# Performance work log

Hardware: AMD Instinct MI355X
Metric: run time of the kernel (lower is better)

Reference implementation:

```python
import jax, jax.numpy as jnp
import numpy as np

N_NODES = 100000
N_EDGES = 1600000
T = 24
F_IN = 16
H = 128
OUT = 64


def setup_inputs() -> dict:
    key = jax.random.key(0)
    ks = jax.random.split(key, 12)
    s = 0.05
    return {
        "x_time_series": jax.random.normal(ks[0], (N_NODES, T, F_IN), jnp.float32),
        "edge_index": jax.random.randint(ks[1], (2, N_EDGES), 0, N_NODES, jnp.int64),
        "gru_W_ih": jax.random.normal(ks[2], (3 * H, F_IN), jnp.float32) * s,
        "gru_W_hh": jax.random.normal(ks[3], (3 * H, H), jnp.float32) * s,
        "gru_b_ih": jax.random.normal(ks[4], (3 * H,), jnp.float32) * s,
        "gru_b_hh": jax.random.normal(ks[5], (3 * H,), jnp.float32) * s,
        "lin1_l_W": jax.random.normal(ks[6], (H, H), jnp.float32) * s,
        "lin1_l_b": jax.random.normal(ks[7], (H,), jnp.float32) * s,
        "lin1_r_W": jax.random.normal(ks[8], (H, H), jnp.float32) * s,
        "lin2_l_W": jax.random.normal(ks[9], (OUT, H), jnp.float32) * s,
        "lin2_l_b": jax.random.normal(ks[10], (OUT,), jnp.float32) * s,
        "lin2_r_W": jax.random.normal(ks[11], (OUT, H), jnp.float32) * s,
    }


def gru_last(x, W_ih, W_hh, b_ih, b_hh):
    # x: [N, T, F]; single-layer batch_first GRU, return last hidden state [N, H]
    Hd = W_hh.shape[1]
    # precompute input projections for all steps: [T, N, 3H]
    gi_all = jnp.einsum('ntf,gf->tng', x, W_ih) + b_ih

    def step(h, gi):
        gh = h @ W_hh.T + b_hh
        r = jax.nn.sigmoid(gi[:, :Hd] + gh[:, :Hd])
        z = jax.nn.sigmoid(gi[:, Hd:2 * Hd] + gh[:, Hd:2 * Hd])
        n = jnp.tanh(gi[:, 2 * Hd:] + r * gh[:, 2 * Hd:])
        h_new = (1.0 - z) * n + z * h
        return h_new, None

    h0 = jnp.zeros((x.shape[0], Hd), x.dtype)
    h_last, _ = jax.lax.scan(step, h0, gi_all)
    return h_last


def sage_conv(x, edge_index, W_l, b_l, W_r):
    # PyG SAGEConv with mean aggregation:
    #   out_i = W_l @ mean_{j->i} x_j + b_l + W_r @ x_i
    src, dst = edge_index[0], edge_index[1]
    n = x.shape[0]
    msg = x[src]                                   # [E, F] irregular gather
    agg = jax.ops.segment_sum(msg, dst, num_segments=n)
    cnt = jax.ops.segment_sum(jnp.ones((msg.shape[0],), x.dtype), dst, num_segments=n)
    mean = agg / jnp.maximum(cnt, 1.0)[:, None]
    return mean @ W_l.T + b_l + x @ W_r.T


def reference(x_time_series, edge_index, gru_W_ih, gru_W_hh, gru_b_ih, gru_b_hh,
              lin1_l_W, lin1_l_b, lin1_r_W, lin2_l_W, lin2_l_b, lin2_r_W):
    x = x_time_series.reshape(-1, T, F_IN)
    h = gru_last(x, gru_W_ih, gru_W_hh, gru_b_ih, gru_b_hh)   # [N, H]
    g = sage_conv(h, edge_index, lin1_l_W, lin1_l_b, lin1_r_W) + h
    g = jax.nn.relu(g)
    # dropout in eval mode -> identity
    out = sage_conv(g, edge_index, lin2_l_W, lin2_l_b, lin2_r_W)
    return out
```

## Files before the change

kernel.cpp:

```cpp
#include <hip/hip_runtime.h>
#include <math.h>

#define NND 100000
#define TT 24
#define FI 16
#define HD 128
#define GD 384
#define OD 64
#define NE 1600000

typedef __bf16 bf16x8 __attribute__((ext_vector_type(8)));
typedef float f32x4 __attribute__((ext_vector_type(4)));
typedef unsigned short u16;
typedef unsigned int u32;

#define S_RZ (-1.44269504f)
#define S_N  (-2.88539008f)

__device__ __forceinline__ u16 f2b(float f) {
    u32 u = __float_as_uint(f);
    u32 r = (u + 0x7FFFu + ((u >> 16) & 1u)) >> 16;
    return (u16)r;
}
__device__ __forceinline__ u32 cvtpk(float lo, float hi) {
    u32 r;
    asm("v_cvt_pk_bf16_f32 %0, %1, %2" : "=v"(r) : "v"(lo), "v"(hi));
    return r;
}
__device__ __forceinline__ float b2f(u16 v) {
    return __uint_as_float((u32)v << 16);
}

__global__ void cvt_x_kernel(const float* __restrict__ x, u16* __restrict__ xb) {
    size_t base = ((size_t)blockIdx.x * 256 + threadIdx.x) * 8;
    float4 a = *(const float4*)(x + base);
    float4 b = *(const float4*)(x + base + 4);
    u32 o0 = cvtpk(a.x, a.y), o1 = cvtpk(a.z, a.w);
    u32 o2 = cvtpk(b.x, b.y), o3 = cvtpk(b.z, b.w);
    *(uint4*)(xb + base) = make_uint4(o0, o1, o2, o3);
}

__global__ void pack_w_kernel(const float* __restrict__ Whh, const float* __restrict__ Wih,
                              const float* __restrict__ bih, const float* __restrict__ bhh,
                              u16* __restrict__ Ap, u16* __restrict__ Aip) {
    int id = blockIdx.x * 256 + threadIdx.x;
    if (id < 6144) {
        int lane = id & 63, fs = id >> 6;
        int s = fs & 3, gt = fs >> 2;
        int row = gt * 16 + (lane & 15);
        float sc = (row < 2 * HD) ? S_RZ : S_N;
        int k0 = s * 32 + (lane >> 4) * 8;
        const float* src = Whh + (size_t)row * HD + k0;
        u16 o[8];
#pragma unroll
        for (int e = 0; e < 8; ++e) o[e] = f2b(src[e] * sc);
        u32* dst = (u32*)(Ap + (size_t)id * 8);
#pragma unroll
        for (int e = 0; e < 4; ++e) dst[e] = (u32)o[2 * e] | ((u32)o[2 * e + 1] << 16);
    } else if (id < 7680) {
        int id2 = id - 6144;
        int lane = id2 & 63, gt = id2 >> 6;
        int row = gt * 16 + (lane & 15);
        float sc = (row < 2 * HD) ? S_RZ : S_N;
        int g = lane >> 4;
        u16 o[8] = {0, 0, 0, 0, 0, 0, 0, 0};
        if (g < 2) {
            const float* src = Wih + (size_t)row * FI + g * 8;
#pragma unroll
            for (int e = 0; e < 8; ++e) o[e] = f2b(src[e] * sc);
        } else if (g == 2) {
            float bias = (row < 2 * HD) ? (bih[row] + bhh[row]) : bih[row];
            o[0] = f2b(bias * sc);
        }
        u32* dst = (u32*)(Aip + (size_t)id2 * 8);
#pragma unroll
        for (int e = 0; e < 4; ++e) dst[e] = (u32)o[2 * e] | ((u32)o[2 * e + 1] << 16);
    }
}

__global__ void pack_gemm_kernel(const float* __restrict__ W, u16* __restrict__ F, int rows) {
    int id = blockIdx.x * 256 + threadIdx.x;
    if (id >= rows * 16) return;
    int lane = id & 63, fs = id >> 6;
    int s = fs & 3, tile = fs >> 2;
    int row = tile * 16 + (lane & 15);
    int k0 = s * 32 + (lane >> 4) * 8;
    const float* src = W + (size_t)row * HD + k0;
    u16 o[8];
#pragma unroll
    for (int e = 0; e < 8; ++e) o[e] = f2b(src[e]);
    u32* dst = (u32*)(F + (size_t)id * 8);
#pragma unroll
    for (int e = 0; e < 4; ++e) dst[e] = (u32)o[2 * e] | ((u32)o[2 * e + 1] << 16);
}

__device__ __forceinline__ int hidx(int row, int col) {
    return row * 128 + (col ^ ((row & 7) << 3));
}

__global__ __launch_bounds__(512) void gru_mfma_kernel(
    const u16* __restrict__ xb,
    const u16* __restrict__ Ap,
    const u16* __restrict__ Aip,
    const float* __restrict__ bhh,
    const u16* __restrict__ Wl,
    const u16* __restrict__ Wr,
    const float* __restrict__ b1,
    u16* __restrict__ P16,
    float* __restrict__ q)
{
    __shared__ u16 hb0[64 * 128];
    __shared__ u16 hb1[64 * 128];

    const int tid = threadIdx.x;
    const int w = tid >> 6, lane = tid & 63;
    const int l15 = lane & 15, g = lane >> 4;
    const int gbase = blockIdx.x * 64;
    const int j0 = w * 16 + g * 4;

    for (int i = tid; i < 64 * 128 / 2; i += 512) ((u32*)hb0)[i] = 0u;

    bf16x8 Ah[3][4], Ai[3];
#pragma unroll
    for (int a = 0; a < 3; ++a) {
        int gt = w + a * 8;
#pragma unroll
        for (int s = 0; s < 4; ++s)
            Ah[a][s] = *(const bf16x8*)(Ap + ((size_t)(gt * 4 + s) * 64 + lane) * 8);
        Ai[a] = *(const bf16x8*)(Aip + ((size_t)gt * 64 + lane) * 8);
    }

    f32x4 bnh4 = *(const f32x4*)(bhh + 256 + j0);
#pragma unroll
    for (int r = 0; r < 4; ++r) bnh4[r] *= S_N;

    const f32x4 fz = {0.f, 0.f, 0.f, 0.f};
    bf16x8 xdef;
    {
        uint4 u = make_uint4(0u, 0u, 0u, 0u);
        if (g == 2) u.x = 0x3F80u;
        *(uint4*)&xdef = u;
    }

    f32x4 hreg[4];
#pragma unroll
    for (int m = 0; m < 4; ++m) hreg[m] = fz;

    int xoff[4];
#pragma unroll
    for (int m = 0; m < 4; ++m) {
        int nd = gbase + m * 16 + l15;
        nd = nd < NND ? nd : NND - 1;
        xoff[m] = nd * (TT * FI) + g * 8;
    }

    __syncthreads();

    auto dostep = [&](int t, const u16* __restrict__ rb, u16* __restrict__ wb) {
#pragma unroll
        for (int mh = 0; mh < 2; ++mh) {
            const int ma = mh * 2, mb = mh * 2 + 1;
            bf16x8 xf0 = xdef, xf1 = xdef;
            if (g < 2) {
                xf0 = *(const bf16x8*)(xb + (size_t)(xoff[ma] + t * FI));
                xf1 = *(const bf16x8*)(xb + (size_t)(xoff[mb] + t * FI));
            }

            const int ra = ma * 16 + l15, rbr = mb * 16 + l15;
            bf16x8 b0[4], b1f[4];
#pragma unroll
            for (int s = 0; s < 4; ++s) {
                b0[s]  = *(const bf16x8*)&rb[hidx(ra, s * 32 + g * 8)];
                b1f[s] = *(const bf16x8*)&rb[hidx(rbr, s * 32 + g * 8)];
            }

            f32x4 acc[3][2], acci[2];
#pragma unroll
            for (int a = 0; a < 3; ++a) {
                acc[a][0] = __builtin_amdgcn_mfma_f32_16x16x32_bf16(Ah[a][0], b0[0], fz, 0, 0, 0);
                acc[a][1] = __builtin_amdgcn_mfma_f32_16x16x32_bf16(Ah[a][0], b1f[0], fz, 0, 0, 0);
            }
#pragma unroll
            for (int s = 1; s < 4; ++s) {
#pragma unroll
                for (int a = 0; a < 3; ++a) {
                    acc[a][0] = __builtin_amdgcn_mfma_f32_16x16x32_bf16(Ah[a][s], b0[s], acc[a][0], 0, 0, 0);
                    acc[a][1] = __builtin_amdgcn_mfma_f32_16x16x32_bf16(Ah[a][s], b1f[s], acc[a][1], 0, 0, 0);
                }
            }
            acc[0][0] = __builtin_amdgcn_mfma_f32_16x16x32_bf16(Ai[0], xf0, acc[0][0], 0, 0, 0);
            acc[1][0] = __builtin_amdgcn_mfma_f32_16x16x32_bf16(Ai[1], xf0, acc[1][0], 0, 0, 0);
            acci[0]   = __builtin_amdgcn_mfma_f32_16x16x32_bf16(Ai[2], xf0, fz, 0, 0, 0);
            acc[0][1] = __builtin_amdgcn_mfma_f32_16x16x32_bf16(Ai[0], xf1, acc[0][1], 0, 0, 0);
            acc[1][1] = __builtin_amdgcn_mfma_f32_16x16x32_bf16(Ai[1], xf1, acc[1][1], 0, 0, 0);
            acci[1]   = __builtin_amdgcn_mfma_f32_16x16x32_bf16(Ai[2], xf1, fz, 0, 0, 0);

#pragma unroll
            for (int mi = 0; mi < 2; ++mi) {
                int m = mh * 2 + mi;
#pragma unroll
                for (int r = 0; r < 4; ++r) {
                    float rr = __builtin_amdgcn_rcpf(1.0f + __builtin_amdgcn_exp2f(acc[0][mi][r]));
                    float zz = __builtin_amdgcn_rcpf(1.0f + __builtin_amdgcn_exp2f(acc[1][mi][r]));
                    float na = acci[mi][r] + rr * (acc[2][mi][r] + bnh4[r]);
                    float nn = 2.0f * __builtin_amdgcn_rcpf(1.0f + __builtin_amdgcn_exp2f(na)) - 1.0f;
                    float h = nn + zz * (hreg[m][r] - nn);
                    hreg[m][r] = h;
                }
                u32 p0 = cvtpk(hreg[m][0], hreg[m][1]);
                u32 p1 = cvtpk(hreg[m][2], hreg[m][3]);
                *(uint2*)&wb[hidx(m * 16 + l15, j0)] = make_uint2(p0, p1);
            }
        }
        __syncthreads();
    };

#pragma unroll 1
    for (int tt = 0; tt < TT; tt += 2) {
        dostep(tt, hb0, hb1);
        dostep(tt + 1, hb1, hb0);
    }

    bf16x8 Al[4], Ar[4];
#pragma unroll
    for (int s = 0; s < 4; ++s) {
        Al[s] = *(const bf16x8*)(Wl + ((size_t)(w * 4 + s) * 64 + lane) * 8);
        Ar[s] = *(const bf16x8*)(Wr + ((size_t)(w * 4 + s) * 64 + lane) * 8);
    }
    f32x4 bq = *(const f32x4*)(b1 + j0);

#pragma unroll
    for (int m = 0; m < 4; ++m) {
        bf16x8 b[4];
#pragma unroll
        for (int s = 0; s < 4; ++s)
            b[s] = *(const bf16x8*)&hb0[hidx(m * 16 + l15, s * 32 + g * 8)];
        f32x4 ap = fz, aq = fz;
#pragma unroll
        for (int s = 0; s < 4; ++s) {
            ap = __builtin_amdgcn_mfma_f32_16x16x32_bf16(Al[s], b[s], ap, 0, 0, 0);
            aq = __builtin_amdgcn_mfma_f32_16x16x32_bf16(Ar[s], b[s], aq, 0, 0, 0);
        }
        int nd = gbase + m * 16 + l15;
        if (nd < NND) {
            u32 c0 = cvtpk(ap[0], ap[1]), c1 = cvtpk(ap[2], ap[3]);
            *(uint2*)(P16 + (size_t)nd * HD + j0) = make_uint2(c0, c1);
            f32x4 v = aq + bq + hreg[m];
            *(f32x4*)(q + (size_t)nd * HD + j0) = v;
        }
    }
}

__global__ void count_kernel(const int* __restrict__ dst, int* __restrict__ cnt) {
    int e = blockIdx.x * 256 + threadIdx.x;
    if (e < NE) atomicAdd(&cnt[dst[e]], 1);
}

__global__ void blocksum_kernel(const int* __restrict__ cnt, int* __restrict__ bsum) {
    __shared__ int sh[256];
    int b = blockIdx.x, t = threadIdx.x;
    int base = b * 1024;
    int s = 0;
    for (int i = t; i < 1024; i += 256) {
        int idx = base + i;
        s += (idx < NND) ? cnt[idx] : 0;
    }
    sh[t] = s; __syncthreads();
    for (int o = 128; o > 0; o >>= 1) { if (t < o) sh[t] += sh[t + o]; __syncthreads(); }
    if (t == 0) bsum[b] = sh[0];
}

__global__ void scanbsum_kernel(int* __restrict__ bsum, int nb, int* __restrict__ rowptr) {
    if (threadIdx.x == 0 && blockIdx.x == 0) {
        int acc = 0;
        for (int i = 0; i < nb; ++i) { int v = bsum[i]; bsum[i] = acc; acc += v; }
        rowptr[NND] = NE;
    }
}

__global__ void scan_kernel(const int* __restrict__ cnt, const int* __restrict__ bsum,
                            int* __restrict__ rowptr) {
    __shared__ int sh[256];
    int b = blockIdx.x, t = threadIdx.x;
    int base = b * 1024;
    int v[4], loc = 0;
#pragma unroll
    for (int j = 0; j < 4; ++j) {
        int idx = base + t * 4 + j;
        v[j] = (idx < NND) ? cnt[idx] : 0;
        loc += v[j];
    }
    sh[t] = loc; __syncthreads();
    for (int o = 1; o < 256; o <<= 1) {
        int x = (t >= o) ? sh[t - o] : 0;
        __syncthreads();
        sh[t] += x;
        __syncthreads();
    }
    int acc = bsum[b] + sh[t] - loc;
#pragma unroll
    for (int j = 0; j < 4; ++j) {
        int idx = base + t * 4 + j;
        if (idx < NND) rowptr[idx] = acc;
        acc += v[j];
    }
}

__global__ void fill_kernel(const int* __restrict__ src, const int* __restrict__ dst,
                            const int* __restrict__ rowptr, int* __restrict__ fill,
                            int* __restrict__ csr) {
    int e = blockIdx.x * 256 + threadIdx.x;
    if (e >= NE) return;
    int d = dst[e];
    int pos = rowptr[d] + atomicAdd(&fill[d], 1);
    csr[pos] = src[e];
}

__global__ __launch_bounds__(512) void gather_proj_kernel(
    const u16* __restrict__ P16,
    const int* __restrict__ rowptr, const int* __restrict__ csr,
    const float* __restrict__ q,
    const u16* __restrict__ W2l, const u16* __restrict__ W2r,
    const float* __restrict__ b2,
    u16* __restrict__ P2,
    float* __restrict__ q2)
{
    __shared__ u16 xs[64 * 128];

    const int tid = threadIdx.x;
    const int w = tid >> 6, lane = tid & 63;
    const int l15 = lane & 15, g = lane >> 4;
    const int gbase = blockIdx.x * 64;
    const f32x4 fz = {0.f, 0.f, 0.f, 0.f};

#pragma unroll 1
    for (int i = 0; i < 8; ++i) {
        int nloc = w * 8 + i;
        int n = gbase + nloc;
        u32 gv = 0u;
        if (n < NND) {
            int beg = rowptr[n], end = rowptr[n + 1];
            float ax = 0.f, ay = 0.f;
            for (int cb = beg; cb < end; cb += 64) {
                int myi = (cb + lane < end) ? csr[cb + lane] : 0;
                int nn = min(end - cb, 64);
                for (int ii = 0; ii < nn; ++ii) {
                    int s = __shfl(myi, ii);
                    u32 pv = *(const u32*)(P16 + (size_t)s * HD + lane * 2);
                    ax += b2f((u16)pv); ay += b2f((u16)(pv >> 16));
                }
            }
            int deg = end - beg;
            float inv = 1.0f / (float)(deg > 0 ? deg : 1);
            float2 qv = *(const float2*)(q + (size_t)n * HD + lane * 2);
            gv = cvtpk(fmaxf(ax * inv + qv.x, 0.f), fmaxf(ay * inv + qv.y, 0.f));
        }
        *(u32*)&xs[hidx(nloc, lane * 2)] = gv;
    }
    __syncthreads();

    const int tile = w & 3;
    const bool isQ = (w >= 4);
    const u16* Wsel = isQ ? W2r : W2l;
    bf16x8 A[4];
#pragma unroll
    for (int s = 0; s < 4; ++s)
        A[s] = *(const bf16x8*)(Wsel + ((size_t)(tile * 4 + s) * 64 + lane) * 8);
    const int f0 = tile * 16 + g * 4;
    f32x4 bq = *(const f32x4*)(b2 + f0);

#pragma unroll
    for (int m = 0; m < 4; ++m) {
        bf16x8 b[4];
#pragma unroll
        for (int s = 0; s < 4; ++s)
            b[s] = *(const bf16x8*)&xs[hidx(m * 16 + l15, s * 32 + g * 8)];
        f32x4 a = fz;
#pragma unroll
        for (int s = 0; s < 4; ++s)
            a = __builtin_amdgcn_mfma_f32_16x16x32_bf16(A[s], b[s], a, 0, 0, 0);
        int nd = gbase + m * 16 + l15;
        if (nd < NND) {
            if (isQ) {
                f32x4 v = a + bq;
                *(f32x4*)(q2 + (size_t)nd * OD + f0) = v;
            } else {
                u32 c0 = cvtpk(a[0], a[1]), c1 = cvtpk(a[2], a[3]);
                *(uint2*)(P2 + (size_t)nd * OD + f0) = make_uint2(c0, c1);
            }
        }
    }
}

__global__ __launch_bounds__(256) void gather2_kernel(
    const u16* __restrict__ P2,
    const int* __restrict__ rowptr, const int* __restrict__ csr,
    const float* __restrict__ q2,
    float* __restrict__ outp)
{
    int n = ((blockIdx.x * 256 + threadIdx.x) >> 6);
    if (n >= NND) return;
    int lane = threadIdx.x & 63;
    int beg = rowptr[n], end = rowptr[n + 1];

    float a = 0.f;
    for (int cb = beg; cb < end; cb += 64) {
        int myi = (cb + lane < end) ? csr[cb + lane] : 0;
        int nn = min(end - cb, 64);
        for (int i = 0; i < nn; ++i) {
            int s = __shfl(myi, i);
            a += b2f(P2[(size_t)s * OD + lane]);
        }
    }
    int deg = end - beg;
    float inv = 1.0f / (float)(deg > 0 ? deg : 1);
    outp[(size_t)n * OD + lane] = a * inv + q2[(size_t)n * OD + lane];
}

extern "C" void kernel_launch(void* const* d_in, const int* in_sizes, int n_in,
                              void* d_out, int out_size, void* d_ws, size_t ws_size,
                              hipStream_t stream) {
    const float* x   = (const float*)d_in[0];
    const int*   edg = (const int*)d_in[1];
    const int*   src = edg;
    const int*   dst = edg + NE;
    const float* Wih = (const float*)d_in[2];
    const float* Whh = (const float*)d_in[3];
    const float* bih = (const float*)d_in[4];
    const float* bhh = (const float*)d_in[5];
    const float* W1l = (const float*)d_in[6];
    const float* b1  = (const float*)d_in[7];
    const float* W1r = (const float*)d_in[8];
    const float* W2l = (const float*)d_in[9];
    const float* b2  = (const float*)d_in[10];
    const float* W2r = (const float*)d_in[11];
    float* out = (float*)d_out;

    char* wsp = (char*)d_ws;
    auto alloc = [&](size_t nbytes) {
        char* p = wsp; wsp += (nbytes + 255) & ~(size_t)255; return p;
    };
    u16*   Ap    = (u16*)alloc((size_t)6144 * 8 * 2);
    u16*   Aip   = (u16*)alloc((size_t)1536 * 8 * 2);
    u16*   Pw1l  = (u16*)alloc((size_t)2048 * 8 * 2);
    u16*   Pw1r  = (u16*)alloc((size_t)2048 * 8 * 2);
    u16*   Pw2l  = (u16*)alloc((size_t)1024 * 8 * 2);
    u16*   Pw2r  = (u16*)alloc((size_t)1024 * 8 * 2);
    int*   cnt   = (int*)alloc((size_t)NND * 4);
    int*   fill  = (int*)alloc((size_t)NND * 4);
    int*   rowp  = (int*)alloc((size_t)(NND + 1) * 4);
    int*   bsum  = (int*)alloc((size_t)128 * 4);
    int*   csr   = (int*)alloc((size_t)NE * 4);
    u16*   xb    = (u16*)alloc((size_t)NND * TT * FI * 2);
    float* q     = (float*)alloc((size_t)NND * HD * 4);
    u16*   P16   = (u16*)alloc((size_t)NND * HD * 2);
    u16*   P2    = (u16*)alloc((size_t)NND * OD * 2);
    float* q2    = (float*)alloc((size_t)NND * OD * 4);

    const int NB_SCAN = (NND + 1023) / 1024;

    hipMemsetAsync(cnt, 0, (size_t)NND * 4, stream);
    hipMemsetAsync(fill, 0, (size_t)NND * 4, stream);

    cvt_x_kernel<<<(NND * TT * FI) / (256 * 8), 256, 0, stream>>>(x, xb);
    pack_w_kernel<<<30, 256, 0, stream>>>(Whh, Wih, bih, bhh, Ap, Aip);
    pack_gemm_kernel<<<8, 256, 0, stream>>>(W1l, Pw1l, HD);
    pack_gemm_kernel<<<8, 256, 0, stream>>>(W1r, Pw1r, HD);
    pack_gemm_kernel<<<4, 256, 0, stream>>>(W2l, Pw2l, OD);
    pack_gemm_kernel<<<4, 256, 0, stream>>>(W2r, Pw2r, OD);

    count_kernel<<<(NE + 255) / 256, 256, 0, stream>>>(dst, cnt);
    blocksum_kernel<<<NB_SCAN, 256, 0, stream>>>(cnt, bsum);
    scanbsum_kernel<<<1, 64, 0, stream>>>(bsum, NB_SCAN, rowp);
    scan_kernel<<<NB_SCAN, 256, 0, stream>>>(cnt, bsum, rowp);
    fill_kernel<<<(NE + 255) / 256, 256, 0, stream>>>(src, dst, rowp, fill, csr);

    const int nblk = (NND + 63) / 64;
    gru_mfma_kernel<<<nblk, 512, 0, stream>>>(xb, Ap, Aip, bhh, Pw1l, Pw1r, b1, P16, q);

    gather_proj_kernel<<<nblk, 512, 0, stream>>>(P16, rowp, csr, q, Pw2l, Pw2r, b2, P2, q2);

    gather2_kernel<<<(NND * 64 + 255) / 256, 256, 0, stream>>>(P2, rowp, csr, q2, out);
}
```

Measured before the change: 831.9 us.

## Restructure GRU step per row tile, batch gather loads, reuse count array for CSR fill

The GRU step now processes one 16-row tile at a time instead of two paired tiles, and the final projection loads each B fragment inside the MFMA loop. Both changes are meant to lower register pressure, at the cost of less instruction-level parallelism per step. The two neighbour-gather kernels issue eight independent loads before accumulating, to hide memory latency in the irregular gather. The CSR fill now decrements the existing count array with atomicSub instead of using a separate zeroed fill array, which removes one memset and one buffer. The order of neighbours within each row changes as a result, so the bf16 summation order also changes.

```diff
diff --git a/kernel.cpp b/kernel.cpp
--- a/kernel.cpp
+++ b/kernel.cpp
@@ -158,59 +158,42 @@
 
     auto dostep = [&](int t, const u16* __restrict__ rb, u16* __restrict__ wb) {
 #pragma unroll
-        for (int mh = 0; mh < 2; ++mh) {
-            const int ma = mh * 2, mb = mh * 2 + 1;
-            bf16x8 xf0 = xdef, xf1 = xdef;
-            if (g < 2) {
-                xf0 = *(const bf16x8*)(xb + (size_t)(xoff[ma] + t * FI));
-                xf1 = *(const bf16x8*)(xb + (size_t)(xoff[mb] + t * FI));
-            }
-
-            const int ra = ma * 16 + l15, rbr = mb * 16 + l15;
-            bf16x8 b0[4], b1f[4];
-#pragma unroll
-            for (int s = 0; s < 4; ++s) {
-                b0[s]  = *(const bf16x8*)&rb[hidx(ra, s * 32 + g * 8)];
-                b1f[s] = *(const bf16x8*)&rb[hidx(rbr, s * 32 + g * 8)];
-            }
-
-            f32x4 acc[3][2], acci[2];
-#pragma unroll
-            for (int a = 0; a < 3; ++a) {
-                acc[a][0] = __builtin_amdgcn_mfma_f32_16x16x32_bf16(Ah[a][0], b0[0], fz, 0, 0, 0);
-                acc[a][1] = __builtin_amdgcn_mfma_f32_16x16x32_bf16(Ah[a][0], b1f[0], fz, 0, 0, 0);
+        for (int m = 0; m < 4; ++m) {
+            bf16x8 xf = xdef;
+            if (g < 2)
+                xf = *(const bf16x8*)(xb + (size_t)(xoff[m] + t * FI));
+
+            const int row = m * 16 + l15;
+            f32x4 a0, a1, a2, ai;
+            {
+                bf16x8 b = *(const bf16x8*)&rb[hidx(row, g * 8)];
+                a0 = __builtin_amdgcn_mfma_f32_16x16x32_bf16(Ah[0][0], b, fz, 0, 0, 0);
+                a1 = __builtin_amdgcn_mfma_f32_16x16x32_bf16(Ah[1][0], b, fz, 0, 0, 0);
+                a2 = __builtin_amdgcn_mfma_f32_16x16x32_bf16(Ah[2][0], b, fz, 0, 0, 0);
             }
 #pragma unroll
             for (int s = 1; s < 4; ++s) {
-#pragma unroll
-                for (int a = 0; a < 3; ++a) {
-                    acc[a][0] = __builtin_amdgcn_mfma_f32_16x16x32_bf16(Ah[a][s], b0[s], acc[a][0], 0, 0, 0);
-                    acc[a][1] = __builtin_amdgcn_mfma_f32_16x16x32_bf16(Ah[a][s], b1f[s], acc[a][1], 0, 0, 0);
-                }
-            }
-            acc[0][0] = __builtin_amdgcn_mfma_f32_16x16x32_bf16(Ai[0], xf0, acc[0][0], 0, 0, 0);
-            acc[1][0] = __builtin_amdgcn_mfma_f32_16x16x32_bf16(Ai[1], xf0, acc[1][0], 0, 0, 0);
-            acci[0]   = __builtin_amdgcn_mfma_f32_16x16x32_bf16(Ai[2], xf0, fz, 0, 0, 0);
-            acc[0][1] = __builtin_amdgcn_mfma_f32_16x16x32_bf16(Ai[0], xf1, acc[0][1], 0, 0, 0);
-            acc[1][1] = __builtin_amdgcn_mfma_f32_16x16x32_bf16(Ai[1], xf1, acc[1][1], 0, 0, 0);
-            acci[1]   = __builtin_amdgcn_mfma_f32_16x16x32_bf16(Ai[2], xf1, fz, 0, 0, 0);
-
-#pragma unroll
-            for (int mi = 0; mi < 2; ++mi) {
-                int m = mh * 2 + mi;
-#pragma unroll
-                for (int r = 0; r < 4; ++r) {
-                    float rr = __builtin_amdgcn_rcpf(1.0f + __builtin_amdgcn_exp2f(acc[0][mi][r]));
-                    float zz = __builtin_amdgcn_rcpf(1.0f + __builtin_amdgcn_exp2f(acc[1][mi][r]));
-                    float na = acci[mi][r] + rr * (acc[2][mi][r] + bnh4[r]);
-                    float nn = 2.0f * __builtin_amdgcn_rcpf(1.0f + __builtin_amdgcn_exp2f(na)) - 1.0f;
-                    float h = nn + zz * (hreg[m][r] - nn);
-                    hreg[m][r] = h;
-                }
-                u32 p0 = cvtpk(hreg[m][0], hreg[m][1]);
-                u32 p1 = cvtpk(hreg[m][2], hreg[m][3]);
-                *(uint2*)&wb[hidx(m * 16 + l15, j0)] = make_uint2(p0, p1);
-            }
+                bf16x8 b = *(const bf16x8*)&rb[hidx(row, s * 32 + g * 8)];
+                a0 = __builtin_amdgcn_mfma_f32_16x16x32_bf16(Ah[0][s], b, a0, 0, 0, 0);
+                a1 = __builtin_amdgcn_mfma_f32_16x16x32_bf16(Ah[1][s], b, a1, 0, 0, 0);
+                a2 = __builtin_amdgcn_mfma_f32_16x16x32_bf16(Ah[2][s], b, a2, 0, 0, 0);
+            }
+            a0 = __builtin_amdgcn_mfma_f32_16x16x32_bf16(Ai[0], xf, a0, 0, 0, 0);
+            a1 = __builtin_amdgcn_mfma_f32_16x16x32_bf16(Ai[1], xf, a1, 0, 0, 0);
+            ai = __builtin_amdgcn_mfma_f32_16x16x32_bf16(Ai[2], xf, fz, 0, 0, 0);
+
+#pragma unroll
+            for (int r = 0; r < 4; ++r) {
+                float rr = __builtin_amdgcn_rcpf(1.0f + __builtin_amdgcn_exp2f(a0[r]));
+                float zz = __builtin_amdgcn_rcpf(1.0f + __builtin_amdgcn_exp2f(a1[r]));
+                float na = ai[r] + rr * (a2[r] + bnh4[r]);
+                float nn = 2.0f * __builtin_amdgcn_rcpf(1.0f + __builtin_amdgcn_exp2f(na)) - 1.0f;
+                float h = nn + zz * (hreg[m][r] - nn);
+                hreg[m][r] = h;
+            }
+            u32 p0 = cvtpk(hreg[m][0], hreg[m][1]);
+            u32 p1 = cvtpk(hreg[m][2], hreg[m][3]);
+            *(uint2*)&wb[hidx(row, j0)] = make_uint2(p0, p1);
         }
         __syncthreads();
     };
@@ -231,15 +214,12 @@
 
 #pragma unroll
     for (int m = 0; m < 4; ++m) {
-        bf16x8 b[4];
-#pragma unroll
-        for (int s = 0; s < 4; ++s)
-            b[s] = *(const bf16x8*)&hb0[hidx(m * 16 + l15, s * 32 + g * 8)];
         f32x4 ap = fz, aq = fz;
 #pragma unroll
         for (int s = 0; s < 4; ++s) {
-            ap = __builtin_amdgcn_mfma_f32_16x16x32_bf16(Al[s], b[s], ap, 0, 0, 0);
-            aq = __builtin_amdgcn_mfma_f32_16x16x32_bf16(Ar[s], b[s], aq, 0, 0, 0);
+            bf16x8 b = *(const bf16x8*)&hb0[hidx(m * 16 + l15, s * 32 + g * 8)];
+            ap = __builtin_amdgcn_mfma_f32_16x16x32_bf16(Al[s], b, ap, 0, 0, 0);
+            aq = __builtin_amdgcn_mfma_f32_16x16x32_bf16(Ar[s], b, aq, 0, 0, 0);
         }
         int nd = gbase + m * 16 + l15;
         if (nd < NND) {
@@ -307,13 +287,13 @@
 }
 
 __global__ void fill_kernel(const int* __restrict__ src, const int* __restrict__ dst,
-                            const int* __restrict__ rowptr, int* __restrict__ fill,
+                            const int* __restrict__ rowptr, int* __restrict__ cnt,
                             int* __restrict__ csr) {
     int e = blockIdx.x * 256 + threadIdx.x;
     if (e >= NE) return;
     int d = dst[e];
-    int pos = rowptr[d] + atomicAdd(&fill[d], 1);
-    csr[pos] = src[e];
+    int off = atomicSub(&cnt[d], 1) - 1;
+    csr[rowptr[d] + off] = src[e];
 }
 
 __global__ __launch_bounds__(512) void gather_proj_kernel(
@@ -344,7 +324,20 @@
             for (int cb = beg; cb < end; cb += 64) {
                 int myi = (cb + lane < end) ? csr[cb + lane] : 0;
                 int nn = min(end - cb, 64);
-                for (int ii = 0; ii < nn; ++ii) {
+                int ii = 0;
+                for (; ii + 8 <= nn; ii += 8) {
+                    u32 p[8];
+#pragma unroll
+                    for (int u = 0; u < 8; ++u) {
+                        int s = __shfl(myi, ii + u);
+                        p[u] = *(const u32*)(P16 + (size_t)s * HD + lane * 2);
+                    }
+#pragma unroll
+                    for (int u = 0; u < 8; ++u) {
+                        ax += b2f((u16)p[u]); ay += b2f((u16)(p[u] >> 16));
+                    }
+                }
+                for (; ii < nn; ++ii) {
                     int s = __shfl(myi, ii);
                     u32 pv = *(const u32*)(P16 + (size_t)s * HD + lane * 2);
                     ax += b2f((u16)pv); ay += b2f((u16)(pv >> 16));
@@ -407,7 +400,18 @@
     for (int cb = beg; cb < end; cb += 64) {
         int myi = (cb + lane < end) ? csr[cb + lane] : 0;
         int nn = min(end - cb, 64);
-        for (int i = 0; i < nn; ++i) {
+        int i = 0;
+        for (; i + 8 <= nn; i += 8) {
+            u16 v[8];
+#pragma unroll
+            for (int u = 0; u < 8; ++u) {
+                int s = __shfl(myi, i + u);
+                v[u] = P2[(size_t)s * OD + lane];
+            }
+#pragma unroll
+            for (int u = 0; u < 8; ++u) a += b2f(v[u]);
+        }
+        for (; i < nn; ++i) {
             int s = __shfl(myi, i);
             a += b2f(P2[(size_t)s * OD + lane]);
         }
@@ -447,7 +451,6 @@
     u16*   Pw2l  = (u16*)alloc((size_t)1024 * 8 * 2);
     u16*   Pw2r  = (u16*)alloc((size_t)1024 * 8 * 2);
     int*   cnt   = (int*)alloc((size_t)NND * 4);
-    int*   fill  = (int*)alloc((size_t)NND * 4);
     int*   rowp  = (int*)alloc((size_t)(NND + 1) * 4);
     int*   bsum  = (int*)alloc((size_t)128 * 4);
     int*   csr   = (int*)alloc((size_t)NE * 4);
@@ -460,7 +463,6 @@
     const int NB_SCAN = (NND + 1023) / 1024;
 
     hipMemsetAsync(cnt, 0, (size_t)NND * 4, stream);
-    hipMemsetAsync(fill, 0, (size_t)NND * 4, stream);
 
     cvt_x_kernel<<<(NND * TT * FI) / (256 * 8), 256, 0, stream>>>(x, xb);
     pack_w_kernel<<<30, 256, 0, stream>>>(Whh, Wih, bih, bhh, Ap, Aip);
@@ -473,7 +475,7 @@
     blocksum_kernel<<<NB_SCAN, 256, 0, stream>>>(cnt, bsum);
     scanbsum_kernel<<<1, 64, 0, stream>>>(bsum, NB_SCAN, rowp);
     scan_kernel<<<NB_SCAN, 256, 0, stream>>>(cnt, bsum, rowp);
-    fill_kernel<<<(NE + 255) / 256, 256, 0, stream>>>(src, dst, rowp, fill, csr);
+    fill_kernel<<<(NE + 255) / 256, 256, 0, stream>>>(src, dst, rowp, cnt, csr);
 
     const int nblk = (NND + 63) / 64;
     gru_mfma_kernel<<<nblk, 512, 0, stream>>>(xb, Ap, Aip, bhh, Pw1l, Pw1r, b1, P16, q);
```

Measured after the change: 746.0 us. 1.12x faster.
